# Kernel tuning notes

Measured on AMD Instinct MI355X. Metric: run time of the kernel, lower is better.

Reference implementation:

```python
import jax, jax.numpy as jnp
import numpy as np

B, L, D_MODEL, H, D_K, D_V = 64, 52, 4096, 32, 128, 128
NEW_C = D_MODEL // H  # per-head input channel after the (faithful) raw reshape


def setup_inputs() -> dict:
    key = jax.random.key(0)
    ks = jax.random.split(key, 12)
    s = 0.02
    return {
        "Q": jax.random.normal(ks[0], (B, L, D_MODEL), jnp.float32),
        "K": jax.random.normal(ks[1], (B, L, D_MODEL), jnp.float32),
        "V": jax.random.normal(ks[2], (B, L, D_MODEL), jnp.float32),
        "Wq": jax.random.normal(ks[3], (H, NEW_C, D_K), jnp.float32) * s,
        "bq": jnp.zeros((H, D_K), jnp.float32),
        "Wk": jax.random.normal(ks[4], (H, NEW_C, D_K), jnp.float32) * s,
        "bk": jnp.zeros((H, D_K), jnp.float32),
        "Wv": jax.random.normal(ks[5], (H, NEW_C, D_V), jnp.float32) * s,
        "bv": jnp.zeros((H, D_V), jnp.float32),
        "Wo": jax.random.normal(ks[6], (H * D_V, D_MODEL), jnp.float32) * s,
        "bo": jnp.zeros((D_MODEL,), jnp.float32),
    }


def reference(Q, K, V, Wq, bq, Wk, bk, Wv, bv, Wo, bo):
    # Faithful to source: raw reshape (B, L, D) -> (B, H, L, D/H), NOT a channel split.
    def split(x):
        return x.reshape(B, H, L, NEW_C)

    q = jnp.einsum('bhlc,hck->bhlk', split(Q), Wq) + bq[None, :, None, :]  # (B,H,L,D_K)
    k = jnp.einsum('bhlc,hck->bhlk', split(K), Wk) + bk[None, :, None, :]
    v = jnp.einsum('bhlc,hcv->bhlv', split(V), Wv) + bv[None, :, None, :]

    scores = jnp.einsum('bhqk,bhmk->bhqm', q, k) / jnp.sqrt(jnp.asarray(D_K, q.dtype))
    # causal mask: keep j <= i, else -inf (matches the numpy masking loop)
    causal = jnp.tril(jnp.ones((L, L), bool))
    scores = jnp.where(causal[None, None], scores, -jnp.inf)
    attn = jax.nn.softmax(scores, axis=-1)
    o = jnp.einsum('bhqm,bhmv->bhqv', attn, v)  # (B,H,L,D_V)
    o = o.transpose(0, 2, 1, 3).reshape(B, L, H * D_V)  # concat heads on last axis
    # Dropout(0.1) is identity at inference.
    return o @ Wo + bo
```

## Files before the change

kernel.cpp:

```cpp
#include <hip/hip_runtime.h>
#include <hip/hip_bf16.h>

#define B_SZ   64
#define L_SZ   52
#define DMODEL 4096
#define H_SZ   32
#define C_SZ   128
#define DK     128

#define GM 3328
#define GN 4096
#define GK 4096

typedef __bf16 bf16x8 __attribute__((ext_vector_type(8)));
typedef float  f32x4  __attribute__((ext_vector_type(4)));

__device__ __forceinline__ void gload_lds16(const void* g, void* l) {
  __builtin_amdgcn_global_load_lds(
      (__attribute__((address_space(1))) void*)(void*)g,
      (__attribute__((address_space(3))) void*)l, 16, 0, 0);
}

__global__ __launch_bounds__(256) void wo_transpose_kernel(
    const float* __restrict__ Wo, __hip_bfloat16* __restrict__ WoT) {
  __shared__ float tile[64][65];
  const int nt = blockIdx.x, mt = blockIdx.y;
  const int t = threadIdx.x;
  const int r  = t >> 4;
  const int c4 = (t & 15) << 2;
#pragma unroll
  for (int p = 0; p < 4; ++p) {
    const int rr = r + p * 16;
    const float4 v = *(const float4*)(Wo + (size_t)(mt * 64 + rr) * 4096 + nt * 64 + c4);
    tile[rr][c4 + 0] = v.x; tile[rr][c4 + 1] = v.y;
    tile[rr][c4 + 2] = v.z; tile[rr][c4 + 3] = v.w;
  }
  __syncthreads();
#pragma unroll
  for (int p = 0; p < 4; ++p) {
    const int rr = r + p * 16;
    union { __hip_bfloat16 h[4]; ushort4 u; } o4;
#pragma unroll
    for (int e = 0; e < 4; ++e) o4.h[e] = __float2bfloat16(tile[c4 + e][rr]);
    *(ushort4*)(WoT + (size_t)(nt * 64 + rr) * 4096 + mt * 64 + c4) = o4.u;
  }
}

__global__ __launch_bounds__(256) void w3_transpose_kernel(
    const float* __restrict__ Wq, const float* __restrict__ Wk,
    const float* __restrict__ Wv, __hip_bfloat16* __restrict__ WqT,
    __hip_bfloat16* __restrict__ WkT, __hip_bfloat16* __restrict__ WvT) {
  __shared__ float tile[64][65];
  const int bz = blockIdx.z;
  const float* in = (bz < 32 ? Wq : (bz < 64 ? Wk : Wv)) + (size_t)(bz & 31) * 16384;
  __hip_bfloat16* out = (bz < 32 ? WqT : (bz < 64 ? WkT : WvT)) + (size_t)(bz & 31) * 16384;
  const int nt = blockIdx.x, mt = blockIdx.y;
  const int t = threadIdx.x;
  const int r  = t >> 4;
  const int c4 = (t & 15) << 2;
#pragma unroll
  for (int p = 0; p < 4; ++p) {
    const int rr = r + p * 16;
    const float4 v = *(const float4*)(in + (size_t)(mt * 64 + rr) * 128 + nt * 64 + c4);
    tile[rr][c4 + 0] = v.x; tile[rr][c4 + 1] = v.y;
    tile[rr][c4 + 2] = v.z; tile[rr][c4 + 3] = v.w;
  }
  __syncthreads();
#pragma unroll
  for (int p = 0; p < 4; ++p) {
    const int rr = r + p * 16;
    union { __hip_bfloat16 h[4]; ushort4 u; } o4;
#pragma unroll
    for (int e = 0; e < 4; ++e) o4.h[e] = __float2bfloat16(tile[c4 + e][rr]);
    *(ushort4*)(out + (size_t)(nt * 64 + rr) * 128 + mt * 64 + c4) = o4.u;
  }
}

template <bool TRANSPOSED>
__device__ __forceinline__ void wave_proj(
    const __hip_bfloat16* __restrict__ xs, const __hip_bfloat16* __restrict__ WT,
    const float* __restrict__ bias, __hip_bfloat16* __restrict__ out,
    int n0, int r16, int kq) {
  f32x4 acc[4][2] = {};
  bf16x8 bfrag[2][4];
#pragma unroll
  for (int nt = 0; nt < 2; ++nt)
#pragma unroll
    for (int kk = 0; kk < 4; ++kk)
      bfrag[nt][kk] = *(const bf16x8*)(WT + (n0 + nt * 16 + r16) * 128 + kk * 32 + kq * 8);
#pragma unroll
  for (int kk = 0; kk < 4; ++kk) {
    bf16x8 a[4];
#pragma unroll
    for (int mt = 0; mt < 4; ++mt)
      a[mt] = *(const bf16x8*)(xs + (mt * 16 + r16) * 136 + kk * 32 + kq * 8);
#pragma unroll
    for (int mt = 0; mt < 4; ++mt)
#pragma unroll
      for (int nt = 0; nt < 2; ++nt)
        acc[mt][nt] = __builtin_amdgcn_mfma_f32_16x16x32_bf16(a[mt], bfrag[nt][kk], acc[mt][nt], 0, 0, 0);
  }
#pragma unroll
  for (int nt = 0; nt < 2; ++nt) {
    const int col = n0 + nt * 16 + r16;
    const float bv = bias[col];
#pragma unroll
    for (int mt = 0; mt < 4; ++mt) {
      const int m0 = mt * 16 + kq * 4;
      if (!TRANSPOSED) {
#pragma unroll
        for (int i = 0; i < 4; ++i)
          out[(m0 + i) * 136 + col] = __float2bfloat16(acc[mt][nt][i] + bv);
      } else {
        union { __hip_bfloat16 h[4]; ushort4 u; } o4;
        if (m0 < 52) {
#pragma unroll
          for (int i = 0; i < 4; ++i) o4.h[i] = __float2bfloat16(acc[mt][nt][i] + bv);
        } else {
          o4.u = make_ushort4(0, 0, 0, 0);
        }
        *(ushort4*)(out + col * 72 + m0) = o4.u;
      }
    }
  }
}

__global__ __launch_bounds__(256, 2) void attn_kernel(
    const float* __restrict__ Qin, const float* __restrict__ Kin,
    const float* __restrict__ Vin,
    const __hip_bfloat16* __restrict__ WqT, const float* __restrict__ bq,
    const __hip_bfloat16* __restrict__ WkT, const float* __restrict__ bk,
    const __hip_bfloat16* __restrict__ WvT, const float* __restrict__ bv,
    __hip_bfloat16* __restrict__ Oc) {
  __shared__ __align__(16) char lds[70656];
  __hip_bfloat16* xs0  = (__hip_bfloat16*)(lds);
  __hip_bfloat16* xs1  = (__hip_bfloat16*)(lds + 17408);
  __hip_bfloat16* xs2  = (__hip_bfloat16*)(lds + 34816);
  __hip_bfloat16* vT   = (__hip_bfloat16*)(lds + 52224);
  __hip_bfloat16* q_sh = (__hip_bfloat16*)(lds + 34816);
  __hip_bfloat16* k_sh = (__hip_bfloat16*)(lds);
  float*          s_sh = (float*)(lds + 17408);
  __hip_bfloat16* p_sh = (__hip_bfloat16*)(lds + 34816);

  const int h = blockIdx.x, bb = blockIdx.y;
  const int t = threadIdx.x;
  const int w = t >> 6, lane = t & 63;
  const int r16 = lane & 15, kq = lane >> 4;
  const size_t xoff = (size_t)bb * (L_SZ * DMODEL) + (size_t)h * (L_SZ * C_SZ);

  {
    const float* xp[3] = {Qin + xoff, Kin + xoff, Vin + xoff};
    __hip_bfloat16* xd[3] = {xs0, xs1, xs2};
#pragma unroll
    for (int tz = 0; tz < 3; ++tz) {
      const float* X = xp[tz];
      __hip_bfloat16* xs = xd[tz];
      for (int idx = t; idx < 52 * 32; idx += 256) {
        const int row = idx >> 5, c4 = (idx & 31) << 2;
        const float4 v = *(const float4*)(X + row * 128 + c4);
        union { __hip_bfloat16 h[4]; ushort4 u; } o4;
        o4.h[0] = __float2bfloat16(v.x); o4.h[1] = __float2bfloat16(v.y);
        o4.h[2] = __float2bfloat16(v.z); o4.h[3] = __float2bfloat16(v.w);
        *(ushort4*)(xs + row * 136 + c4) = o4.u;
      }
      if (t < 12 * 17) {
        const int row = 52 + t / 17, c8 = (t % 17) * 8;
        *(uint4*)(xs + row * 136 + c8) = make_uint4(0, 0, 0, 0);
      }
    }
  }
  __syncthreads();

  wave_proj<true>(xs2, WvT + (size_t)h * 16384, bv + h * 128, vT, w * 32, r16, kq);
  __syncthreads();
  wave_proj<false>(xs0, WqT + (size_t)h * 16384, bq + h * 128, q_sh, w * 32, r16, kq);
  __syncthreads();
  wave_proj<false>(xs1, WkT + (size_t)h * 16384, bk + h * 128, k_sh, w * 32, r16, kq);
  __syncthreads();

  {
    const int n0 = w * 16;
    f32x4 sacc[4] = {};
#pragma unroll
    for (int kk = 0; kk < 4; ++kk) {
      const bf16x8 bf_ = *(const bf16x8*)(k_sh + (n0 + r16) * 136 + kk * 32 + kq * 8);
#pragma unroll
      for (int mt = 0; mt < 4; ++mt) {
        const bf16x8 a = *(const bf16x8*)(q_sh + (mt * 16 + r16) * 136 + kk * 32 + kq * 8);
        sacc[mt] = __builtin_amdgcn_mfma_f32_16x16x32_bf16(a, bf_, sacc[mt], 0, 0, 0);
      }
    }
    const float scale = 0.08838834764831845f;
#pragma unroll
    for (int mt = 0; mt < 4; ++mt)
#pragma unroll
      for (int i = 0; i < 4; ++i)
        s_sh[(mt * 16 + kq * 4 + i) * 68 + n0 + r16] = sacc[mt][i] * scale;
  }
  __syncthreads();

  {
    const int r = t >> 2, qd = t & 3;
    if (r < 52) {
      float v[16];
      float mx = -3e38f;
#pragma unroll
      for (int j4 = 0; j4 < 4; ++j4) {
        const f32x4 s4 = *(const f32x4*)(s_sh + r * 68 + qd * 16 + j4 * 4);
#pragma unroll
        for (int e = 0; e < 4; ++e) {
          const int col = qd * 16 + j4 * 4 + e;
          const float val = (col <= r) ? s4[e] : -3e38f;
          v[j4 * 4 + e] = val;
          mx = fmaxf(mx, val);
        }
      }
      mx = fmaxf(mx, __shfl_xor(mx, 1));
      mx = fmaxf(mx, __shfl_xor(mx, 2));
      float ex[16];
      float sum = 0.f;
#pragma unroll
      for (int j = 0; j < 16; ++j) {
        const int col = qd * 16 + j;
        const float e = (col <= r) ? __expf(v[j] - mx) : 0.f;
        ex[j] = e; sum += e;
      }
      sum += __shfl_xor(sum, 1);
      sum += __shfl_xor(sum, 2);
      const float inv = 1.0f / sum;
      union { __hip_bfloat16 h[8]; uint4 q; } p0, p1;
#pragma unroll
      for (int j = 0; j < 8; ++j) {
        p0.h[j] = __float2bfloat16(ex[j] * inv);
        p1.h[j] = __float2bfloat16(ex[8 + j] * inv);
      }
      *(uint4*)(p_sh + r * 72 + qd * 16)     = p0.q;
      *(uint4*)(p_sh + r * 72 + qd * 16 + 8) = p1.q;
    } else {
      *(uint4*)(p_sh + r * 72 + qd * 16)     = make_uint4(0, 0, 0, 0);
      *(uint4*)(p_sh + r * 72 + qd * 16 + 8) = make_uint4(0, 0, 0, 0);
    }
  }
  __syncthreads();

  {
    const int n0 = w * 32;
    f32x4 oacc[4][2] = {};
#pragma unroll
    for (int kk = 0; kk < 2; ++kk) {
      bf16x8 bfr[2];
#pragma unroll
      for (int nt = 0; nt < 2; ++nt)
        bfr[nt] = *(const bf16x8*)(vT + (n0 + nt * 16 + r16) * 72 + kk * 32 + kq * 8);
#pragma unroll
      for (int mt = 0; mt < 4; ++mt) {
        const bf16x8 a = *(const bf16x8*)(p_sh + (mt * 16 + r16) * 72 + kk * 32 + kq * 8);
#pragma unroll
        for (int nt = 0; nt < 2; ++nt)
          oacc[mt][nt] = __builtin_amdgcn_mfma_f32_16x16x32_bf16(a, bfr[nt], oacc[mt][nt], 0, 0, 0);
      }
    }
    const size_t obase = (size_t)bb * 52 * 4096 + (size_t)h * 128;
#pragma unroll
    for (int nt = 0; nt < 2; ++nt) {
      const int col = n0 + nt * 16 + r16;
#pragma unroll
      for (int mt = 0; mt < 4; ++mt) {
        const int row0 = mt * 16 + kq * 4;
#pragma unroll
        for (int i = 0; i < 4; ++i) {
          const int row = row0 + i;
          if (row < 52)
            Oc[obase + (size_t)row * 4096 + col] = __float2bfloat16(oacc[mt][nt][i]);
        }
      }
    }
  }
}

#define STAGE(GBASE, REGOFF, KT, KS, WB) do {                                  \
    const __hip_bfloat16* s_ = (GBASE) + (size_t)(KT) * 64 + (KS) * 32;        \
    char* d_ = (WB) + (REGOFF) + ((KS) ? 16384 : 0) + t * 16;                  \
    gload_lds16(s_, d_);                                                       \
    gload_lds16(s_ + (size_t)128 * GK, d_ + 8192);                             \
  } while (0)

#define WAIT_LGKM0()                                                           \
  asm volatile("s_waitcnt lgkmcnt(0)" ::: "memory");                           \
  __builtin_amdgcn_sched_barrier(0)

#define LOAD_AF(DST, BASE)                                                     \
  _Pragma("unroll")                                                            \
  for (int mf = 0; mf < 4; ++mf)                                               \
    DST[mf] = *(const bf16x8*)((BASE) + mf * 1024)

#define LOAD_BF(DST, BASE)                                                     \
  _Pragma("unroll")                                                            \
  for (int nf = 0; nf < 4; ++nf)                                               \
    DST[nf] = *(const bf16x8*)((BASE) + nf * 1024)

#define CLUSTER(AF, BF, MQ)                                                    \
  __builtin_amdgcn_sched_barrier(0);                                           \
  __builtin_amdgcn_s_setprio(1);                                               \
  _Pragma("unroll")                                                            \
  for (int mf = 0; mf < 4; ++mf)                                               \
    _Pragma("unroll")                                                          \
    for (int nf = 0; nf < 4; ++nf)                                             \
      acc[(MQ) * 4 + mf][nf] = __builtin_amdgcn_mfma_f32_16x16x32_bf16(        \
          AF[mf], BF[nf], acc[(MQ) * 4 + mf][nf], 0, 0, 0);                    \
  __builtin_amdgcn_s_setprio(0)

__global__ __launch_bounds__(512, 2) void out_gemm_kernel(
    const __hip_bfloat16* __restrict__ A, const __hip_bfloat16* __restrict__ Bt,
    const float* __restrict__ bias, float* __restrict__ C) {
  __shared__ __align__(16) char lds[131072];

  int bid = blockIdx.x;
  bid = (bid & 7) * 26 + (bid >> 3);
  const int tm = bid >> 4;
  const int tn = bid & 15;

  const int t = threadIdx.x;
  const int w = t >> 6, lane = t & 63;
  const int wm = w >> 2, wn = w & 3;
  const int r16 = lane & 15, kq = lane >> 4;

  const int srow = t >> 2;
  const int sgslot = (t & 3) ^ ((srow >> 1) & 3);
  const __hip_bfloat16* gA0 = A  + (size_t)(tm * 256 + srow) * GK + sgslot * 8;
  const __hip_bfloat16* gB0 = Bt + (size_t)(tn * 256 + srow) * GK + sgslot * 8;

  const int slotr = kq ^ ((r16 >> 1) & 3);
  const int aB0 = (wm * 128 + r16) * 64 + slotr * 16;
  const int bB  = 32768 + (wn * 64 + r16) * 64 + slotr * 16;

  f32x4 acc[8][4] = {};
  bf16x8 af0[4], af1[4], bf0[4], bf1[4];

  STAGE(gA0, 0,     0, 0, lds);
  STAGE(gA0, 0,     0, 1, lds);
  STAGE(gB0, 32768, 0, 0, lds);
  STAGE(gB0, 32768, 0, 1, lds);
  STAGE(gA0, 0,     1, 0, lds + 65536);
  STAGE(gA0, 0,     1, 1, lds + 65536);
  STAGE(gB0, 32768, 1, 0, lds + 65536);
  STAGE(gB0, 32768, 1, 1, lds + 65536);
  asm volatile("s_waitcnt vmcnt(8)" ::: "memory");
  __builtin_amdgcn_s_barrier();
  LOAD_AF(af0, lds + aB0);
  LOAD_BF(bf0, lds + bB);

#pragma unroll 1
  for (int kt = 0; kt < 64; ++kt) {
    char* rb = lds + ((kt & 1) << 16);
    char* nb = lds + (((kt + 1) & 1) << 16);

    WAIT_LGKM0();
    LOAD_AF(af1, rb + 4096 + aB0);
    CLUSTER(af0, bf0, 0);

    WAIT_LGKM0();
    LOAD_AF(af0, rb + 16384 + aB0);
    LOAD_BF(bf1, rb + 16384 + bB);
    CLUSTER(af1, bf0, 1);

    WAIT_LGKM0();
    LOAD_AF(af1, rb + 16384 + 4096 + aB0);
    CLUSTER(af0, bf1, 0);

    WAIT_LGKM0();
    __builtin_amdgcn_s_barrier();
    {
      const int st2 = kt + 2 < 64 ? kt + 2 : 63;
      STAGE(gA0, 0,     st2, 0, rb);
      STAGE(gA0, 0,     st2, 1, rb);
      STAGE(gB0, 32768, st2, 0, rb);
      STAGE(gB0, 32768, st2, 1, rb);
    }
    asm volatile("s_waitcnt vmcnt(8)" ::: "memory");
    __builtin_amdgcn_s_barrier();
    LOAD_AF(af0, nb + aB0);
    LOAD_BF(bf0, nb + bB);
    CLUSTER(af1, bf1, 1);
  }
  asm volatile("s_waitcnt vmcnt(0) lgkmcnt(0)" ::: "memory");

  const int row0 = tm * 256 + wm * 128 + kq * 4;
  const int col0 = tn * 256 + wn * 64 + r16;
#pragma unroll
  for (int nf = 0; nf < 4; ++nf) {
    const int col = col0 + nf * 16;
    const float bv = bias[col];
#pragma unroll
    for (int mf = 0; mf < 8; ++mf) {
      const int row = row0 + mf * 16;
#pragma unroll
      for (int i = 0; i < 4; ++i)
        C[(size_t)(row + i) * GN + col] = acc[mf][nf][i] + bv;
    }
  }
}

extern "C" void kernel_launch(void* const* d_in, const int* in_sizes, int n_in,
                              void* d_out, int out_size, void* d_ws, size_t ws_size,
                              hipStream_t stream) {
  const float* Q  = (const float*)d_in[0];
  const float* K  = (const float*)d_in[1];
  const float* V  = (const float*)d_in[2];
  const float* Wq = (const float*)d_in[3];
  const float* bq = (const float*)d_in[4];
  const float* Wk = (const float*)d_in[5];
  const float* bk = (const float*)d_in[6];
  const float* Wv = (const float*)d_in[7];
  const float* bv = (const float*)d_in[8];
  const float* Wo = (const float*)d_in[9];
  const float* bo = (const float*)d_in[10];
  float* out = (float*)d_out;

  char* wsb = (char*)d_ws;
  __hip_bfloat16* WoT = (__hip_bfloat16*)wsb;
  __hip_bfloat16* Oc  = (__hip_bfloat16*)(wsb + (size_t)GN * GK * 2);
  __hip_bfloat16* WqT = (__hip_bfloat16*)(wsb + (size_t)GN * GK * 2 + (size_t)GM * GN * 2);
  __hip_bfloat16* WkT = WqT + (size_t)H_SZ * C_SZ * DK;
  __hip_bfloat16* WvT = WkT + (size_t)H_SZ * C_SZ * DK;

  w3_transpose_kernel<<<dim3(2, 2, 96), 256, 0, stream>>>(Wq, Wk, Wv, WqT, WkT, WvT);
  wo_transpose_kernel<<<dim3(64, 64), 256, 0, stream>>>(Wo, WoT);
  attn_kernel<<<dim3(H_SZ, B_SZ), 256, 0, stream>>>(Q, K, V, WqT, bq, WkT, bk, WvT, bv, Oc);
  out_gemm_kernel<<<dim3(13 * 16), 512, 0, stream>>>(Oc, WoT, bo, out);
}
```

Before: 230.9 us.

## Interleave global-to-LDS staging across four MFMA clusters in output GEMM

After: 216.7 us. 1.07x faster.

```diff
diff --git a/kernel.cpp b/kernel.cpp
--- a/kernel.cpp
+++ b/kernel.cpp
@@ -285,21 +285,7 @@
     gload_lds16(s_ + (size_t)128 * GK, d_ + 8192);                             \
   } while (0)
 
-#define WAIT_LGKM0()                                                           \
-  asm volatile("s_waitcnt lgkmcnt(0)" ::: "memory");                           \
-  __builtin_amdgcn_sched_barrier(0)
-
-#define LOAD_AF(DST, BASE)                                                     \
-  _Pragma("unroll")                                                            \
-  for (int mf = 0; mf < 4; ++mf)                                               \
-    DST[mf] = *(const bf16x8*)((BASE) + mf * 1024)
-
-#define LOAD_BF(DST, BASE)                                                     \
-  _Pragma("unroll")                                                            \
-  for (int nf = 0; nf < 4; ++nf)                                               \
-    DST[nf] = *(const bf16x8*)((BASE) + nf * 1024)
-
-#define CLUSTER(AF, BF, MQ)                                                    \
+#define MFMA16(MQ, BF)                                                         \
   __builtin_amdgcn_sched_barrier(0);                                           \
   __builtin_amdgcn_s_setprio(1);                                               \
   _Pragma("unroll")                                                            \
@@ -307,8 +293,18 @@
     _Pragma("unroll")                                                          \
     for (int nf = 0; nf < 4; ++nf)                                             \
       acc[(MQ) * 4 + mf][nf] = __builtin_amdgcn_mfma_f32_16x16x32_bf16(        \
-          AF[mf], BF[nf], acc[(MQ) * 4 + mf][nf], 0, 0, 0);                    \
+          af[mf], BF[nf], acc[(MQ) * 4 + mf][nf], 0, 0, 0);                    \
   __builtin_amdgcn_s_setprio(0)
+
+#define READ_AF(KS, MQ)                                                        \
+  _Pragma("unroll")                                                            \
+  for (int mf = 0; mf < 4; ++mf)                                               \
+    af[mf] = *(const bf16x8*)(rb + (KS) * 16384 + (MQ) * 4096 + aB0 + mf * 1024)
+
+#define READ_BF(BF, KS)                                                        \
+  _Pragma("unroll")                                                            \
+  for (int nf = 0; nf < 4; ++nf)                                               \
+    BF[nf] = *(const bf16x8*)(rb + 32768 + (KS) * 16384 + bB0 + nf * 1024)
 
 __global__ __launch_bounds__(512, 2) void out_gemm_kernel(
     const __hip_bfloat16* __restrict__ A, const __hip_bfloat16* __restrict__ Bt,
@@ -332,56 +328,67 @@
 
   const int slotr = kq ^ ((r16 >> 1) & 3);
   const int aB0 = (wm * 128 + r16) * 64 + slotr * 16;
-  const int bB  = 32768 + (wn * 64 + r16) * 64 + slotr * 16;
+  const int bB0 = (wn * 64 + r16) * 64 + slotr * 16;
 
   f32x4 acc[8][4] = {};
-  bf16x8 af0[4], af1[4], bf0[4], bf1[4];
+  bf16x8 bf0[4], bf1[4];
 
   STAGE(gA0, 0,     0, 0, lds);
   STAGE(gA0, 0,     0, 1, lds);
   STAGE(gB0, 32768, 0, 0, lds);
   STAGE(gB0, 32768, 0, 1, lds);
+  STAGE(gB0, 32768, 1, 0, lds + 65536);
   STAGE(gA0, 0,     1, 0, lds + 65536);
-  STAGE(gA0, 0,     1, 1, lds + 65536);
-  STAGE(gB0, 32768, 1, 0, lds + 65536);
   STAGE(gB0, 32768, 1, 1, lds + 65536);
-  asm volatile("s_waitcnt vmcnt(8)" ::: "memory");
+  asm volatile("s_waitcnt vmcnt(6)" ::: "memory");
   __builtin_amdgcn_s_barrier();
-  LOAD_AF(af0, lds + aB0);
-  LOAD_BF(bf0, lds + bB);
 
 #pragma unroll 1
   for (int kt = 0; kt < 64; ++kt) {
     char* rb = lds + ((kt & 1) << 16);
-    char* nb = lds + (((kt + 1) & 1) << 16);
-
-    WAIT_LGKM0();
-    LOAD_AF(af1, rb + 4096 + aB0);
-    CLUSTER(af0, bf0, 0);
-
-    WAIT_LGKM0();
-    LOAD_AF(af0, rb + 16384 + aB0);
-    LOAD_BF(bf1, rb + 16384 + bB);
-    CLUSTER(af1, bf0, 1);
-
-    WAIT_LGKM0();
-    LOAD_AF(af1, rb + 16384 + 4096 + aB0);
-    CLUSTER(af0, bf1, 0);
-
-    WAIT_LGKM0();
-    __builtin_amdgcn_s_barrier();
+    char* ob = lds + (((kt + 1) & 1) << 16);
+    const int s1 = kt + 1 < 64 ? kt + 1 : 63;
+    const int s2 = kt + 2 < 64 ? kt + 2 : 63;
+
     {
-      const int st2 = kt + 2 < 64 ? kt + 2 : 63;
-      STAGE(gA0, 0,     st2, 0, rb);
-      STAGE(gA0, 0,     st2, 1, rb);
-      STAGE(gB0, 32768, st2, 0, rb);
-      STAGE(gB0, 32768, st2, 1, rb);
-    }
-    asm volatile("s_waitcnt vmcnt(8)" ::: "memory");
-    __builtin_amdgcn_s_barrier();
-    LOAD_AF(af0, nb + aB0);
-    LOAD_BF(bf0, nb + bB);
-    CLUSTER(af1, bf1, 1);
+      bf16x8 af[4];
+      READ_AF(0, 0);
+      READ_BF(bf0, 0);
+      STAGE(gA0, 0, s1, 1, ob);
+      __builtin_amdgcn_s_barrier();
+      asm volatile("s_waitcnt lgkmcnt(0)" ::: "memory");
+      MFMA16(0, bf0);
+      __builtin_amdgcn_s_barrier();
+    }
+    {
+      bf16x8 af[4];
+      READ_AF(0, 1);
+      STAGE(gB0, 32768, s2, 0, rb);
+      __builtin_amdgcn_s_barrier();
+      asm volatile("s_waitcnt lgkmcnt(0)" ::: "memory");
+      MFMA16(1, bf0);
+      __builtin_amdgcn_s_barrier();
+    }
+    {
+      bf16x8 af[4];
+      READ_AF(1, 0);
+      READ_BF(bf1, 1);
+      STAGE(gA0, 0, s2, 0, rb);
+      __builtin_amdgcn_s_barrier();
+      asm volatile("s_waitcnt lgkmcnt(0)" ::: "memory");
+      MFMA16(0, bf1);
+      __builtin_amdgcn_s_barrier();
+    }
+    {
+      bf16x8 af[4];
+      READ_AF(1, 1);
+      STAGE(gB0, 32768, s2, 1, rb);
+      __builtin_amdgcn_s_barrier();
+      asm volatile("s_waitcnt lgkmcnt(0)" ::: "memory");
+      MFMA16(1, bf1);
+      asm volatile("s_waitcnt vmcnt(6)" ::: "memory");
+      __builtin_amdgcn_s_barrier();
+    }
   }
   asm volatile("s_waitcnt vmcnt(0) lgkmcnt(0)" ::: "memory");
 
```
